# Kernel optimization log

Measured on AMD Instinct MI355X. Metric: run time of the kernel, lower is better.

## Reference

```python
import jax, jax.numpy as jnp
import numpy as np

EPS = 1e-6
B, N, K = 4, 65536, 16
D_IN, D_OUT, DH = 8, 16, 8  # DH = d_out // 2


def _bn(x, g, b):
    # train-mode BatchNorm2d over (B, N, K) per channel (channels-last here)
    m = jnp.mean(x, axis=(0, 1, 2))
    v = jnp.var(x, axis=(0, 1, 2))
    return (x - m) * jax.lax.rsqrt(v + EPS) * g + b


def _conv(x, w, b):
    # 1x1 Conv2d == per-point linear; x: (B,N,K,Cin), w: (Cout,Cin)
    return jnp.einsum('bnki,oi->bnko', x, w) + b


def _lse(coords, feats, idx, w, b, g, bt):
    # coords: (B,N,3), feats: (B,N,1,D), idx: (B,N,K)
    nbrs = jnp.take_along_axis(coords[:, :, None, :], idx[:, :, :, None], axis=1)  # (B,N,K,3)
    ctr = jnp.broadcast_to(coords[:, :, None, :], nbrs.shape)
    dist = jnp.ones(idx.shape + (1,), dtype=coords.dtype)  # torch path passes idx only -> dist = ones
    enc = jnp.concatenate([ctr, nbrs, ctr - nbrs, dist], axis=-1)  # (B,N,K,10)
    h = jax.nn.relu(_bn(_conv(enc, w, b), g, bt))
    f = jnp.broadcast_to(feats, idx.shape + (feats.shape[-1],))
    return jnp.concatenate([h, f], axis=-1)  # (B,N,K,2*D)


def _pool(x, sw, w, b, g, bt):
    # attentive pooling: softmax over neighbor axis K (axis=2)
    scores = jax.nn.softmax(jnp.einsum('bnki,oi->bnko', x, sw), axis=2)
    agg = jnp.sum(scores * x, axis=2, keepdims=True)  # (B,N,1,C)
    return jax.nn.relu(_bn(_conv(agg, w, b), g, bt))


def setup_inputs() -> dict:
    key = jax.random.key(0)
    ks = jax.random.split(key, 16)
    rn = lambda k, s: (0.1 * jax.random.normal(k, s)).astype(jnp.float32)
    inp = {
        'coords': jax.random.normal(ks[0], (B, N, 3), dtype=jnp.float32),
        'features': jax.random.normal(ks[1], (B, D_IN, N, 1), dtype=jnp.float32),
        'idx': jax.random.randint(ks[2], (B, N, K), 0, N, dtype=jnp.int32),
        # mlp1: d_in -> d_out//2, no bn, LeakyReLU(0.2)
        'w1': rn(ks[3], (DH, D_IN)), 'b1': jnp.zeros((DH,), jnp.float32),
        # lse1 mlp: 10 -> d_out//2, bn + ReLU
        'lse1_w': rn(ks[4], (DH, 10)), 'lse1_b': jnp.zeros((DH,), jnp.float32),
        'lse1_g': jnp.ones((DH,), jnp.float32), 'lse1_bt': jnp.zeros((DH,), jnp.float32),
        # pool1: in d_out -> out d_out//2
        'p1_sw': rn(ks[5], (D_OUT, D_OUT)),
        'p1_w': rn(ks[6], (DH, D_OUT)), 'p1_b': jnp.zeros((DH,), jnp.float32),
        'p1_g': jnp.ones((DH,), jnp.float32), 'p1_bt': jnp.zeros((DH,), jnp.float32),
        # lse2
        'lse2_w': rn(ks[7], (DH, 10)), 'lse2_b': jnp.zeros((DH,), jnp.float32),
        'lse2_g': jnp.ones((DH,), jnp.float32), 'lse2_bt': jnp.zeros((DH,), jnp.float32),
        # pool2: in d_out -> out d_out
        'p2_sw': rn(ks[8], (D_OUT, D_OUT)),
        'p2_w': rn(ks[9], (D_OUT, D_OUT)), 'p2_b': jnp.zeros((D_OUT,), jnp.float32),
        'p2_g': jnp.ones((D_OUT,), jnp.float32), 'p2_bt': jnp.zeros((D_OUT,), jnp.float32),
        # mlp2: d_out -> 2*d_out (no bn/act)
        'w2': rn(ks[10], (2 * D_OUT, D_OUT)), 'b2': jnp.zeros((2 * D_OUT,), jnp.float32),
        # shortcut: d_in -> 2*d_out, bn, no act
        'sc_w': rn(ks[11], (2 * D_OUT, D_IN)), 'sc_b': jnp.zeros((2 * D_OUT,), jnp.float32),
        'sc_g': jnp.ones((2 * D_OUT,), jnp.float32), 'sc_bt': jnp.zeros((2 * D_OUT,), jnp.float32),
    }
    return inp


def reference(coords, features, idx, w1, b1, lse1_w, lse1_b, lse1_g, lse1_bt,
              p1_sw, p1_w, p1_b, p1_g, p1_bt, lse2_w, lse2_b, lse2_g, lse2_bt,
              p2_sw, p2_w, p2_b, p2_g, p2_bt, w2, b2, sc_w, sc_b, sc_g, sc_bt):
    feats = jnp.transpose(features, (0, 2, 3, 1))  # (B,N,1,d_in) channels-last
    x = jax.nn.leaky_relu(_conv(feats, w1, b1), 0.2)           # (B,N,1,DH)
    x = _lse(coords, x, idx, lse1_w, lse1_b, lse1_g, lse1_bt)  # (B,N,K,D_OUT)
    x = _pool(x, p1_sw, p1_w, p1_b, p1_g, p1_bt)               # (B,N,1,DH)
    x = _lse(coords, x, idx, lse2_w, lse2_b, lse2_g, lse2_bt)  # (B,N,K,D_OUT)
    x = _pool(x, p2_sw, p2_w, p2_b, p2_g, p2_bt)               # (B,N,1,D_OUT)
    out = jax.nn.leaky_relu(
        _conv(x, w2, b2) + _bn(_conv(feats, sc_w, sc_b), sc_g, sc_bt), 0.01)
    return jnp.transpose(out, (0, 3, 1, 2))  # (B, 2*d_out, N, 1)
```

## Files before the change

kernel.cpp:

```cpp
#include <hip/hip_runtime.h>

#define NB 4
#define NN 65536
#define NK 16
#define NP (NB * NN)
#define BN_EPS 1e-6f
#define LOG2E 1.44269504088896f

#define WS_ENC_M   0
#define WS_SC_M    32
#define WS_S_Y2    96
#define WS_SS_Y2   104
#define WS_S_Y4    112
#define WS_SS_Y4   128
#define WS_Y2      1024
#define WS_Y4      (1024 + NP * 8)
#define WS_C4      (1024 + NP * 24)
#define WS_NB      (1024 + NP * 28)

template <int NCH>
__device__ inline void blockReduceAtomic(float (&v)[NCH], float* __restrict__ dst) {
    __shared__ float red[4][NCH];
    const int lane = threadIdx.x & 63;
    const int wv = threadIdx.x >> 6;
    __syncthreads();
#pragma unroll
    for (int c = 0; c < NCH; c++) {
        float x = v[c];
#pragma unroll
        for (int off = 32; off > 0; off >>= 1) x += __shfl_xor(x, off, 64);
        if (lane == 0) red[wv][c] = x;
    }
    __syncthreads();
    for (int c = threadIdx.x; c < NCH; c += 256)
        atomicAdd(dst + c, red[0][c] + red[1][c] + red[2][c] + red[3][c]);
    __syncthreads();
}

__device__ inline void bn_from_enc(const float* __restrict__ M, const float* __restrict__ w,
                                   float b, float g, float bt, float& sc, float& sh) {
    float u[6];
    u[0] = w[0] + w[6]; u[1] = w[1] + w[7]; u[2] = w[2] + w[8];
    u[3] = w[3] - w[6]; u[4] = w[4] - w[7]; u[5] = w[5] - w[8];
    const float beta = b + w[9];
    float lin = 0.f;
#pragma unroll
    for (int i = 0; i < 6; i++) lin += u[i] * M[i];
    float quad = u[0] * u[0] * M[6] + 2.f * u[0] * u[1] * M[7] + 2.f * u[0] * u[2] * M[8]
               + u[1] * u[1] * M[9] + 2.f * u[1] * u[2] * M[10] + u[2] * u[2] * M[11];
#pragma unroll
    for (int i = 0; i < 3; i++)
#pragma unroll
        for (int j = 0; j < 3; j++) quad += 2.f * u[i] * u[3 + j] * M[12 + i * 3 + j];
    quad += u[3] * u[3] * M[21] + 2.f * u[3] * u[4] * M[22] + 2.f * u[3] * u[5] * M[23]
          + u[4] * u[4] * M[24] + 2.f * u[4] * u[5] * M[25] + u[5] * u[5] * M[26];
    const float cnt = (float)NP * (float)NK;
    const float sum = lin + cnt * beta;
    const float ss = quad + 2.f * beta * lin + cnt * beta * beta;
    const float m = sum / cnt, v = ss / cnt - m * m;
    sc = g * rsqrtf(v + BN_EPS);
    sh = bt - m * sc;
}

__global__ __launch_bounds__(256) void k_pack(
    const float* __restrict__ coords, const float* __restrict__ feats,
    float4* __restrict__ c4, float* __restrict__ ws) {
    const int tid = threadIdx.x;
    const int p = blockIdx.x * 256 + tid;
    const int b = p >> 16;
    const int n = p & (NN - 1);
    c4[p] = make_float4(coords[3 * p], coords[3 * p + 1], coords[3 * p + 2], 0.f);
    float accf[44];
    float f[8];
#pragma unroll
    for (int i = 0; i < 8; i++) f[i] = feats[(b * 8 + i) * NN + n];
#pragma unroll
    for (int i = 0; i < 8; i++) accf[i] = f[i];
    int t2 = 8;
#pragma unroll
    for (int i = 0; i < 8; i++)
#pragma unroll
        for (int j = i; j < 8; j++) accf[t2++] = f[i] * f[j];
    blockReduceAtomic<44>(accf, ws + WS_SC_M);
}

__global__ __launch_bounds__(256) void k_stats(
    const float4* __restrict__ c4, const int* __restrict__ idx,
    float* __restrict__ ws) {
    const int tid = threadIdx.x;
    const int p = blockIdx.x * 256 + tid;
    const int b = p >> 16;
    const int boff = b << 16;
    float* __restrict__ nbp = ws + WS_NB;
    const int4* ip = (const int4*)idx + p * 4;
    const float4 me = c4[p];

    float sn0 = 0.f, sn1 = 0.f, sn2 = 0.f;
    float m00 = 0.f, m01 = 0.f, m02 = 0.f, m11 = 0.f, m12 = 0.f, m22 = 0.f;

    auto emit = [&](int k, const float4 nn) {
        nbp[(3 * k    ) * NP + p] = nn.x;
        nbp[(3 * k + 1) * NP + p] = nn.y;
        nbp[(3 * k + 2) * NP + p] = nn.z;
        sn0 += nn.x; sn1 += nn.y; sn2 += nn.z;
        m00 += nn.x * nn.x; m01 += nn.x * nn.y; m02 += nn.x * nn.z;
        m11 += nn.y * nn.y; m12 += nn.y * nn.z; m22 += nn.z * nn.z;
    };

    int4 v = ip[0];
    float4 n0 = c4[boff + v.x], n1 = c4[boff + v.y], n2 = c4[boff + v.z], n3 = c4[boff + v.w];
#pragma unroll 1
    for (int q = 0; q < 3; q++) {
        const int4 vn = ip[q + 1];
        const float4 t0 = c4[boff + vn.x], t1 = c4[boff + vn.y],
                     t2 = c4[boff + vn.z], t3 = c4[boff + vn.w];
        emit(4 * q, n0); emit(4 * q + 1, n1); emit(4 * q + 2, n2); emit(4 * q + 3, n3);
        n0 = t0; n1 = t1; n2 = t2; n3 = t3;
    }
    emit(12, n0); emit(13, n1); emit(14, n2); emit(15, n3);

    float acc[27];
    acc[0] = 16.f * me.x; acc[1] = 16.f * me.y; acc[2] = 16.f * me.z;
    acc[3] = sn0; acc[4] = sn1; acc[5] = sn2;
    acc[6] = 16.f * me.x * me.x; acc[7] = 16.f * me.x * me.y; acc[8] = 16.f * me.x * me.z;
    acc[9] = 16.f * me.y * me.y; acc[10] = 16.f * me.y * me.z; acc[11] = 16.f * me.z * me.z;
    acc[12] = me.x * sn0; acc[13] = me.x * sn1; acc[14] = me.x * sn2;
    acc[15] = me.y * sn0; acc[16] = me.y * sn1; acc[17] = me.y * sn2;
    acc[18] = me.z * sn0; acc[19] = me.z * sn1; acc[20] = me.z * sn2;
    acc[21] = m00; acc[22] = m01; acc[23] = m02;
    acc[24] = m11; acc[25] = m12; acc[26] = m22;
    blockReduceAtomic<27>(acc, ws + WS_ENC_M);
}

__global__ __launch_bounds__(256) void k_pool1(
    const float4* __restrict__ c4, const float* __restrict__ feats,
    const float* __restrict__ w1, const float* __restrict__ b1,
    const float* __restrict__ lse1_w, const float* __restrict__ lse1_b,
    const float* __restrict__ lse1_g, const float* __restrict__ lse1_bt,
    const float* __restrict__ lse2_w, const float* __restrict__ lse2_b,
    const float* __restrict__ lse2_g, const float* __restrict__ lse2_bt,
    const float* __restrict__ p1_sw, const float* __restrict__ p1_w,
    const float* __restrict__ p1_b,
    const float* __restrict__ p2_sw, const float* __restrict__ p2_w,
    const float* __restrict__ p2_b, float* __restrict__ ws) {
    __shared__ float an1[24], dcA[24], dkA[8], an2[24], dcB[24], dkB[8],
        sws1[64], sws2[64], pws1[128], pws2[256], pbs1[8], pbs2[16], w1s[64], b1s[8];
    const int tid = threadIdx.x;
    if (tid < 8) {
        const int c = tid;
        {
            const float* w = lse1_w + c * 10;
            float sc, sh;
            bn_from_enc(ws + WS_ENC_M, w, lse1_b[c], lse1_g[c], lse1_bt[c], sc, sh);
#pragma unroll
            for (int i = 0; i < 3; i++) {
                an1[c * 3 + i] = sc * (w[3 + i] - w[6 + i]);
                dcA[c * 3 + i] = sc * (w[i] + w[6 + i]);
            }
            dkA[c] = sc * (lse1_b[c] + w[9]) + sh;
        }
        {
            const float* w = lse2_w + c * 10;
            float sc, sh;
            bn_from_enc(ws + WS_ENC_M, w, lse2_b[c], lse2_g[c], lse2_bt[c], sc, sh);
#pragma unroll
            for (int i = 0; i < 3; i++) {
                an2[c * 3 + i] = sc * (w[3 + i] - w[6 + i]);
                dcB[c * 3 + i] = sc * (w[i] + w[6 + i]);
            }
            dkB[c] = sc * (lse2_b[c] + w[9]) + sh;
        }
        b1s[c] = b1[c]; pbs1[c] = p1_b[c];
    }
    if (tid < 16) pbs2[tid] = p2_b[tid];
    if (tid < 64) {
        w1s[tid] = w1[tid];
        sws1[tid] = p1_sw[(tid >> 3) * 16 + (tid & 7)] * LOG2E;
        sws2[tid] = p2_sw[(tid >> 3) * 16 + (tid & 7)] * LOG2E;
    }
    if (tid < 128) pws1[tid] = p1_w[tid];
    if (tid < 256) pws2[tid] = p2_w[tid];
    __syncthreads();

    const int p = blockIdx.x * 256 + tid;
    const int b = p >> 16;
    const int n = p & (NN - 1);
    const float* __restrict__ nbp = ws + WS_NB;
    const float4 me = c4[p];
    float d1[8], d2[8];
#pragma unroll
    for (int c = 0; c < 8; c++) {
        d1[c] = dcA[c * 3] * me.x + dcA[c * 3 + 1] * me.y + dcA[c * 3 + 2] * me.z + dkA[c];
        d2[c] = dcB[c * 3] * me.x + dcB[c * 3 + 1] * me.y + dcB[c * 3 + 2] * me.z + dkB[c];
    }
    float l1[8] = {}, a1[8] = {}, l2[8] = {}, a2[8] = {};

    auto proc = [&](float nx, float ny, float nz) {
        float h[8];
#pragma unroll
        for (int c = 0; c < 8; c++) {
            float y = an1[c * 3] * nx + an1[c * 3 + 1] * ny + an1[c * 3 + 2] * nz + d1[c];
            h[c] = y > 0.f ? y : 0.f;
        }
#pragma unroll
        for (int o = 0; o < 8; o++) {
            float s = 0.f;
#pragma unroll
            for (int i = 0; i < 8; i++) s += h[i] * sws1[o * 8 + i];
            float e2 = exp2f(s);
            l1[o] += e2; a1[o] += e2 * h[o];
        }
#pragma unroll
        for (int c = 0; c < 8; c++) {
            float y = an2[c * 3] * nx + an2[c * 3 + 1] * ny + an2[c * 3 + 2] * nz + d2[c];
            h[c] = y > 0.f ? y : 0.f;
        }
#pragma unroll
        for (int o = 0; o < 8; o++) {
            float s = 0.f;
#pragma unroll
            for (int i = 0; i < 8; i++) s += h[i] * sws2[o * 8 + i];
            float e2 = exp2f(s);
            l2[o] += e2; a2[o] += e2 * h[o];
        }
    };

    float X[4], Y[4], Z[4];
#pragma unroll
    for (int e = 0; e < 4; e++) {
        X[e] = nbp[(3 * e    ) * NP + p];
        Y[e] = nbp[(3 * e + 1) * NP + p];
        Z[e] = nbp[(3 * e + 2) * NP + p];
    }
#pragma unroll 1
    for (int q = 0; q < 3; q++) {
        float TX[4], TY[4], TZ[4];
#pragma unroll
        for (int e = 0; e < 4; e++) {
            const int k = 4 * (q + 1) + e;
            TX[e] = nbp[(3 * k    ) * NP + p];
            TY[e] = nbp[(3 * k + 1) * NP + p];
            TZ[e] = nbp[(3 * k + 2) * NP + p];
        }
#pragma unroll
        for (int e = 0; e < 4; e++) proc(X[e], Y[e], Z[e]);
#pragma unroll
        for (int e = 0; e < 4; e++) { X[e] = TX[e]; Y[e] = TY[e]; Z[e] = TZ[e]; }
    }
#pragma unroll
    for (int e = 0; e < 4; e++) proc(X[e], Y[e], Z[e]);

    float f[8];
#pragma unroll
    for (int i = 0; i < 8; i++) f[i] = feats[(b * 8 + i) * NN + n];
    float agg[16];
#pragma unroll
    for (int o = 0; o < 8; o++) agg[o] = a1[o] * __builtin_amdgcn_rcpf(l1[o]);
#pragma unroll
    for (int jq = 0; jq < 8; jq++) {
        float y = b1s[jq];
#pragma unroll
        for (int i = 0; i < 8; i++) y += f[i] * w1s[jq * 8 + i];
        agg[8 + jq] = y > 0.f ? y : 0.2f * y;
    }
    float st[16];
#pragma unroll
    for (int c = 0; c < 8; c++) {
        float y = pbs1[c];
#pragma unroll
        for (int o = 0; o < 16; o++) y += agg[o] * pws1[c * 16 + o];
        ws[WS_Y2 + c * NP + p] = y;
        st[c] = y; st[8 + c] = y * y;
    }
    float g2[8];
#pragma unroll
    for (int o = 0; o < 8; o++) g2[o] = a2[o] * __builtin_amdgcn_rcpf(l2[o]);
#pragma unroll
    for (int c = 0; c < 16; c++) {
        float y = pbs2[c];
#pragma unroll
        for (int o = 0; o < 8; o++) y += g2[o] * pws2[c * 16 + o];
        ws[WS_Y4 + c * NP + p] = y;
    }
    blockReduceAtomic<16>(st, ws + WS_S_Y2);
}

__global__ __launch_bounds__(256) void k_pool2e(
    const float* __restrict__ p1_g, const float* __restrict__ p1_bt,
    const float* __restrict__ p2_w, float* __restrict__ ws) {
    __shared__ float p1sc[8], p1sh[8], pwsb[128];
    const int tid = threadIdx.x;
    if (tid < 8) {
        const int c = tid;
        const float cP = 1.f / (float)NP;
        float m = ws[WS_S_Y2 + c] * cP, vv = ws[WS_SS_Y2 + c] * cP - m * m;
        float sc = p1_g[c] * rsqrtf(vv + BN_EPS);
        p1sc[c] = sc; p1sh[c] = p1_bt[c] - m * sc;
    }
    if (tid < 128) pwsb[tid] = p2_w[(tid >> 3) * 16 + 8 + (tid & 7)];
    __syncthreads();

    const int p = blockIdx.x * 256 + tid;
    float x2[8];
#pragma unroll
    for (int c = 0; c < 8; c++) {
        float y = ws[WS_Y2 + c * NP + p] * p1sc[c] + p1sh[c];
        x2[c] = y > 0.f ? y : 0.f;
    }
    float st[32];
#pragma unroll
    for (int c = 0; c < 16; c++) {
        float y = ws[WS_Y4 + c * NP + p];
#pragma unroll
        for (int o = 0; o < 8; o++) y += x2[o] * pwsb[c * 8 + o];
        ws[WS_Y4 + c * NP + p] = y;
        st[c] = y; st[16 + c] = y * y;
    }
    blockReduceAtomic<32>(st, ws + WS_S_Y4);
}

__global__ __launch_bounds__(256) void k_final(
    const float* __restrict__ feats, const float* __restrict__ w2,
    const float* __restrict__ b2, const float* __restrict__ sc_w,
    const float* __restrict__ sc_b, const float* __restrict__ p2_g,
    const float* __restrict__ p2_bt, const float* __restrict__ sc_g,
    const float* __restrict__ sc_bt, const float* __restrict__ ws,
    float* __restrict__ out) {
    __shared__ float w2s[512], b2s[32], scws[256], scbs[32],
        p2sc[16], p2sh[16], scsc[32], scsh[32];
    const int tid = threadIdx.x;
    for (int i = tid; i < 512; i += 256) w2s[i] = w2[i];
    if (tid < 256) scws[tid] = sc_w[tid];
    if (tid < 32) {
        b2s[tid] = b2[tid]; scbs[tid] = sc_b[tid];
        const int c = tid;
        const float* w = sc_w + c * 8;
        const float* S = ws + WS_SC_M;
        float lin = 0.f;
#pragma unroll
        for (int i = 0; i < 8; i++) lin += w[i] * S[i];
        float quad = 0.f;
        int t2 = 0;
#pragma unroll
        for (int i = 0; i < 8; i++)
#pragma unroll
            for (int j = i; j < 8; j++) {
                const float mm = S[8 + t2++];
                quad += (i == j ? 1.f : 2.f) * w[i] * w[j] * mm;
            }
        const float cnt = (float)NP;
        const float bb = sc_b[c];
        const float sum = lin + cnt * bb;
        const float ss = quad + 2.f * bb * lin + cnt * bb * bb;
        const float m = sum / cnt, vv = ss / cnt - m * m;
        const float sc = sc_g[c] * rsqrtf(vv + BN_EPS);
        scsc[c] = sc; scsh[c] = sc_bt[c] - m * sc;
    }
    if (tid < 16) {
        const int c = tid;
        const float cP = 1.f / (float)NP;
        float m = ws[WS_S_Y4 + c] * cP, vv = ws[WS_SS_Y4 + c] * cP - m * m;
        float sc = p2_g[c] * rsqrtf(vv + BN_EPS);
        p2sc[c] = sc; p2sh[c] = p2_bt[c] - m * sc;
    }
    __syncthreads();

    const int p = blockIdx.x * 256 + tid;
    const int b = p >> 16;
    const int n = p & (NN - 1);
    float x4[16];
#pragma unroll
    for (int c = 0; c < 16; c++) {
        float y = ws[WS_Y4 + c * NP + p] * p2sc[c] + p2sh[c];
        x4[c] = y > 0.f ? y : 0.f;
    }
    float f[8];
#pragma unroll
    for (int i = 0; i < 8; i++) f[i] = feats[(b * 8 + i) * NN + n];
#pragma unroll
    for (int c = 0; c < 32; c++) {
        float s = scbs[c];
#pragma unroll
        for (int i = 0; i < 8; i++) s += f[i] * scws[c * 8 + i];
        s = s * scsc[c] + scsh[c];
        float m = b2s[c];
#pragma unroll
        for (int o = 0; o < 16; o++) m += x4[o] * w2s[c * 16 + o];
        float vv = m + s;
        out[(b * 32 + c) * NN + n] = vv > 0.f ? vv : 0.01f * vv;
    }
}

extern "C" void kernel_launch(void* const* d_in, const int* in_sizes, int n_in,
                              void* d_out, int out_size, void* d_ws, size_t ws_size,
                              hipStream_t stream) {
    (void)in_sizes; (void)n_in; (void)out_size; (void)ws_size;
    const float* coords = (const float*)d_in[0];
    const float* features = (const float*)d_in[1];
    const int* idx = (const int*)d_in[2];
    const float* w1 = (const float*)d_in[3];
    const float* b1 = (const float*)d_in[4];
    const float* lse1_w = (const float*)d_in[5];
    const float* lse1_b = (const float*)d_in[6];
    const float* lse1_g = (const float*)d_in[7];
    const float* lse1_bt = (const float*)d_in[8];
    const float* p1_sw = (const float*)d_in[9];
    const float* p1_w = (const float*)d_in[10];
    const float* p1_b = (const float*)d_in[11];
    const float* p1_g = (const float*)d_in[12];
    const float* p1_bt = (const float*)d_in[13];
    const float* lse2_w = (const float*)d_in[14];
    const float* lse2_b = (const float*)d_in[15];
    const float* lse2_g = (const float*)d_in[16];
    const float* lse2_bt = (const float*)d_in[17];
    const float* p2_sw = (const float*)d_in[18];
    const float* p2_w = (const float*)d_in[19];
    const float* p2_b = (const float*)d_in[20];
    const float* p2_g = (const float*)d_in[21];
    const float* p2_bt = (const float*)d_in[22];
    const float* w2 = (const float*)d_in[23];
    const float* b2 = (const float*)d_in[24];
    const float* sc_w = (const float*)d_in[25];
    const float* sc_b = (const float*)d_in[26];
    const float* sc_g = (const float*)d_in[27];
    const float* sc_bt = (const float*)d_in[28];
    float* ws = (float*)d_ws;
    float* out = (float*)d_out;
    float4* c4 = (float4*)(ws + WS_C4);

    const int NBLK = NP / 256;
    (void)hipMemsetAsync(ws, 0, 144 * sizeof(float), stream);
    k_pack<<<NBLK, 256, 0, stream>>>(coords, features, c4, ws);
    k_stats<<<NBLK, 256, 0, stream>>>(c4, idx, ws);
    k_pool1<<<NBLK, 256, 0, stream>>>(c4, features, w1, b1,
                                      lse1_w, lse1_b, lse1_g, lse1_bt,
                                      lse2_w, lse2_b, lse2_g, lse2_bt,
                                      p1_sw, p1_w, p1_b, p2_sw, p2_w, p2_b, ws);
    k_pool2e<<<NBLK, 256, 0, stream>>>(p1_g, p1_bt, p2_w, ws);
    k_final<<<NBLK, 256, 0, stream>>>(features, w2, b2, sc_w, sc_b, p2_g, p2_bt,
                                      sc_g, sc_bt, ws, out);
}
```

Before: 339.4 us.

## Split fused pool kernel into two passes and pack workspace as float4

The combined pool kernel, which evaluated both LSE/attention branches per neighbor, is split into two kernels that each handle one branch, with launch bounds requesting higher occupancy. The gathered neighbor coordinates and the Y2/Y4 intermediates are repacked so each thread moves 16-byte float4s instead of scalar channel planes. exp2f is replaced by the hardware exp2 builtin. In exchange, the neighbor buffer is read twice and an extra launch is added, aiming to cut register pressure and memory instructions.

```diff
diff --git a/kernel.cpp b/kernel.cpp
--- a/kernel.cpp
+++ b/kernel.cpp
@@ -13,10 +13,10 @@
 #define WS_SS_Y2   104
 #define WS_S_Y4    112
 #define WS_SS_Y4   128
-#define WS_Y2      1024
-#define WS_Y4      (1024 + NP * 8)
-#define WS_C4      (1024 + NP * 24)
-#define WS_NB      (1024 + NP * 28)
+#define WS_C4      1024
+#define WS_NB4     (1024 + NP * 4)
+#define WS_Y2      (1024 + NP * 52)
+#define WS_Y4      (1024 + NP * 60)
 
 template <int NCH>
 __device__ inline void blockReduceAtomic(float (&v)[NCH], float* __restrict__ dst) {
@@ -91,20 +91,23 @@
     const int p = blockIdx.x * 256 + tid;
     const int b = p >> 16;
     const int boff = b << 16;
-    float* __restrict__ nbp = ws + WS_NB;
+    float4* __restrict__ nb4 = (float4*)(ws + WS_NB4);
     const int4* ip = (const int4*)idx + p * 4;
     const float4 me = c4[p];
 
     float sn0 = 0.f, sn1 = 0.f, sn2 = 0.f;
     float m00 = 0.f, m01 = 0.f, m02 = 0.f, m11 = 0.f, m12 = 0.f, m22 = 0.f;
 
-    auto emit = [&](int k, const float4 nn) {
-        nbp[(3 * k    ) * NP + p] = nn.x;
-        nbp[(3 * k + 1) * NP + p] = nn.y;
-        nbp[(3 * k + 2) * NP + p] = nn.z;
+    auto mom = [&](const float4 nn) {
         sn0 += nn.x; sn1 += nn.y; sn2 += nn.z;
         m00 += nn.x * nn.x; m01 += nn.x * nn.y; m02 += nn.x * nn.z;
         m11 += nn.y * nn.y; m12 += nn.y * nn.z; m22 += nn.z * nn.z;
+    };
+    auto emitq = [&](int q, const float4 n0, const float4 n1, const float4 n2, const float4 n3) {
+        nb4[(3 * q    ) * NP + p] = make_float4(n0.x, n0.y, n0.z, n1.x);
+        nb4[(3 * q + 1) * NP + p] = make_float4(n1.y, n1.z, n2.x, n2.y);
+        nb4[(3 * q + 2) * NP + p] = make_float4(n2.z, n3.x, n3.y, n3.z);
+        mom(n0); mom(n1); mom(n2); mom(n3);
     };
 
     int4 v = ip[0];
@@ -114,10 +117,10 @@
         const int4 vn = ip[q + 1];
         const float4 t0 = c4[boff + vn.x], t1 = c4[boff + vn.y],
                      t2 = c4[boff + vn.z], t3 = c4[boff + vn.w];
-        emit(4 * q, n0); emit(4 * q + 1, n1); emit(4 * q + 2, n2); emit(4 * q + 3, n3);
+        emitq(q, n0, n1, n2, n3);
         n0 = t0; n1 = t1; n2 = t2; n3 = t3;
     }
-    emit(12, n0); emit(13, n1); emit(14, n2); emit(15, n3);
+    emitq(3, n0, n1, n2, n3);
 
     float acc[27];
     acc[0] = 16.f * me.x; acc[1] = 16.f * me.y; acc[2] = 16.f * me.z;
@@ -132,68 +135,45 @@
     blockReduceAtomic<27>(acc, ws + WS_ENC_M);
 }
 
-__global__ __launch_bounds__(256) void k_pool1(
+__global__ __launch_bounds__(256, 3) void k_pool1a(
     const float4* __restrict__ c4, const float* __restrict__ feats,
     const float* __restrict__ w1, const float* __restrict__ b1,
     const float* __restrict__ lse1_w, const float* __restrict__ lse1_b,
     const float* __restrict__ lse1_g, const float* __restrict__ lse1_bt,
-    const float* __restrict__ lse2_w, const float* __restrict__ lse2_b,
-    const float* __restrict__ lse2_g, const float* __restrict__ lse2_bt,
     const float* __restrict__ p1_sw, const float* __restrict__ p1_w,
-    const float* __restrict__ p1_b,
-    const float* __restrict__ p2_sw, const float* __restrict__ p2_w,
-    const float* __restrict__ p2_b, float* __restrict__ ws) {
-    __shared__ float an1[24], dcA[24], dkA[8], an2[24], dcB[24], dkB[8],
-        sws1[64], sws2[64], pws1[128], pws2[256], pbs1[8], pbs2[16], w1s[64], b1s[8];
+    const float* __restrict__ p1_b, float* __restrict__ ws) {
+    __shared__ float an1[24], dcA[24], dkA[8], sws1[64], pws1[128], pbs1[8], w1s[64], b1s[8];
     const int tid = threadIdx.x;
     if (tid < 8) {
         const int c = tid;
-        {
-            const float* w = lse1_w + c * 10;
-            float sc, sh;
-            bn_from_enc(ws + WS_ENC_M, w, lse1_b[c], lse1_g[c], lse1_bt[c], sc, sh);
-#pragma unroll
-            for (int i = 0; i < 3; i++) {
-                an1[c * 3 + i] = sc * (w[3 + i] - w[6 + i]);
-                dcA[c * 3 + i] = sc * (w[i] + w[6 + i]);
-            }
-            dkA[c] = sc * (lse1_b[c] + w[9]) + sh;
-        }
-        {
-            const float* w = lse2_w + c * 10;
-            float sc, sh;
-            bn_from_enc(ws + WS_ENC_M, w, lse2_b[c], lse2_g[c], lse2_bt[c], sc, sh);
-#pragma unroll
-            for (int i = 0; i < 3; i++) {
-                an2[c * 3 + i] = sc * (w[3 + i] - w[6 + i]);
-                dcB[c * 3 + i] = sc * (w[i] + w[6 + i]);
-            }
-            dkB[c] = sc * (lse2_b[c] + w[9]) + sh;
-        }
+        const float* w = lse1_w + c * 10;
+        float sc, sh;
+        bn_from_enc(ws + WS_ENC_M, w, lse1_b[c], lse1_g[c], lse1_bt[c], sc, sh);
+#pragma unroll
+        for (int i = 0; i < 3; i++) {
+            an1[c * 3 + i] = sc * (w[3 + i] - w[6 + i]);
+            dcA[c * 3 + i] = sc * (w[i] + w[6 + i]);
+        }
+        dkA[c] = sc * (lse1_b[c] + w[9]) + sh;
         b1s[c] = b1[c]; pbs1[c] = p1_b[c];
     }
-    if (tid < 16) pbs2[tid] = p2_b[tid];
     if (tid < 64) {
         w1s[tid] = w1[tid];
         sws1[tid] = p1_sw[(tid >> 3) * 16 + (tid & 7)] * LOG2E;
-        sws2[tid] = p2_sw[(tid >> 3) * 16 + (tid & 7)] * LOG2E;
     }
     if (tid < 128) pws1[tid] = p1_w[tid];
-    if (tid < 256) pws2[tid] = p2_w[tid];
     __syncthreads();
 
     const int p = blockIdx.x * 256 + tid;
     const int b = p >> 16;
     const int n = p & (NN - 1);
-    const float* __restrict__ nbp = ws + WS_NB;
+    const float4* __restrict__ nb4 = (const float4*)(ws + WS_NB4);
     const float4 me = c4[p];
-    float d1[8], d2[8];
-#pragma unroll
-    for (int c = 0; c < 8; c++) {
+    float d1[8];
+#pragma unroll
+    for (int c = 0; c < 8; c++)
         d1[c] = dcA[c * 3] * me.x + dcA[c * 3 + 1] * me.y + dcA[c * 3 + 2] * me.z + dkA[c];
-        d2[c] = dcB[c * 3] * me.x + dcB[c * 3 + 1] * me.y + dcB[c * 3 + 2] * me.z + dkB[c];
-    }
-    float l1[8] = {}, a1[8] = {}, l2[8] = {}, a2[8] = {};
+    float l1[8] = {}, a1[8] = {};
 
     auto proc = [&](float nx, float ny, float nz) {
         float h[8];
@@ -207,9 +187,88 @@
             float s = 0.f;
 #pragma unroll
             for (int i = 0; i < 8; i++) s += h[i] * sws1[o * 8 + i];
-            float e2 = exp2f(s);
+            float e2 = __builtin_amdgcn_exp2f(s);
             l1[o] += e2; a1[o] += e2 * h[o];
         }
+    };
+    auto proc4 = [&](const float4 c0, const float4 c1, const float4 c2) {
+        proc(c0.x, c0.y, c0.z); proc(c0.w, c1.x, c1.y);
+        proc(c1.z, c1.w, c2.x); proc(c2.y, c2.z, c2.w);
+    };
+
+    float4 A0 = nb4[0 * NP + p], A1 = nb4[1 * NP + p], A2 = nb4[2 * NP + p];
+#pragma unroll 1
+    for (int g = 0; g < 3; g++) {
+        const float4 B0 = nb4[(3 * g + 3) * NP + p], B1 = nb4[(3 * g + 4) * NP + p],
+                     B2 = nb4[(3 * g + 5) * NP + p];
+        proc4(A0, A1, A2);
+        A0 = B0; A1 = B1; A2 = B2;
+    }
+    proc4(A0, A1, A2);
+
+    float f[8];
+#pragma unroll
+    for (int i = 0; i < 8; i++) f[i] = feats[(b * 8 + i) * NN + n];
+    float agg[16];
+#pragma unroll
+    for (int o = 0; o < 8; o++) agg[o] = a1[o] * __builtin_amdgcn_rcpf(l1[o]);
+#pragma unroll
+    for (int jq = 0; jq < 8; jq++) {
+        float y = b1s[jq];
+#pragma unroll
+        for (int i = 0; i < 8; i++) y += f[i] * w1s[jq * 8 + i];
+        agg[8 + jq] = y > 0.f ? y : 0.2f * y;
+    }
+    float st[16], yv[8];
+#pragma unroll
+    for (int c = 0; c < 8; c++) {
+        float y = pbs1[c];
+#pragma unroll
+        for (int o = 0; o < 16; o++) y += agg[o] * pws1[c * 16 + o];
+        yv[c] = y; st[c] = y; st[8 + c] = y * y;
+    }
+    float4* __restrict__ y2 = (float4*)(ws + WS_Y2);
+    y2[0 * NP + p] = make_float4(yv[0], yv[1], yv[2], yv[3]);
+    y2[1 * NP + p] = make_float4(yv[4], yv[5], yv[6], yv[7]);
+    blockReduceAtomic<16>(st, ws + WS_S_Y2);
+}
+
+__global__ __launch_bounds__(256, 3) void k_pool1b(
+    const float4* __restrict__ c4,
+    const float* __restrict__ lse2_w, const float* __restrict__ lse2_b,
+    const float* __restrict__ lse2_g, const float* __restrict__ lse2_bt,
+    const float* __restrict__ p2_sw, const float* __restrict__ p2_w,
+    const float* __restrict__ p2_b, float* __restrict__ ws) {
+    __shared__ float an2[24], dcB[24], dkB[8], sws2[64], pws2h[128], pbs2[16];
+    const int tid = threadIdx.x;
+    if (tid < 8) {
+        const int c = tid;
+        const float* w = lse2_w + c * 10;
+        float sc, sh;
+        bn_from_enc(ws + WS_ENC_M, w, lse2_b[c], lse2_g[c], lse2_bt[c], sc, sh);
+#pragma unroll
+        for (int i = 0; i < 3; i++) {
+            an2[c * 3 + i] = sc * (w[3 + i] - w[6 + i]);
+            dcB[c * 3 + i] = sc * (w[i] + w[6 + i]);
+        }
+        dkB[c] = sc * (lse2_b[c] + w[9]) + sh;
+    }
+    if (tid < 16) pbs2[tid] = p2_b[tid];
+    if (tid < 64) sws2[tid] = p2_sw[(tid >> 3) * 16 + (tid & 7)] * LOG2E;
+    if (tid < 128) pws2h[tid] = p2_w[(tid >> 3) * 16 + (tid & 7)];
+    __syncthreads();
+
+    const int p = blockIdx.x * 256 + tid;
+    const float4* __restrict__ nb4 = (const float4*)(ws + WS_NB4);
+    const float4 me = c4[p];
+    float d2[8];
+#pragma unroll
+    for (int c = 0; c < 8; c++)
+        d2[c] = dcB[c * 3] * me.x + dcB[c * 3 + 1] * me.y + dcB[c * 3 + 2] * me.z + dkB[c];
+    float l2[8] = {}, a2[8] = {};
+
+    auto proc = [&](float nx, float ny, float nz) {
+        float h[8];
 #pragma unroll
         for (int c = 0; c < 8; c++) {
             float y = an2[c * 3] * nx + an2[c * 3 + 1] * ny + an2[c * 3 + 2] * nz + d2[c];
@@ -220,69 +279,42 @@
             float s = 0.f;
 #pragma unroll
             for (int i = 0; i < 8; i++) s += h[i] * sws2[o * 8 + i];
-            float e2 = exp2f(s);
+            float e2 = __builtin_amdgcn_exp2f(s);
             l2[o] += e2; a2[o] += e2 * h[o];
         }
     };
-
-    float X[4], Y[4], Z[4];
-#pragma unroll
-    for (int e = 0; e < 4; e++) {
-        X[e] = nbp[(3 * e    ) * NP + p];
-        Y[e] = nbp[(3 * e + 1) * NP + p];
-        Z[e] = nbp[(3 * e + 2) * NP + p];
-    }
+    auto proc4 = [&](const float4 c0, const float4 c1, const float4 c2) {
+        proc(c0.x, c0.y, c0.z); proc(c0.w, c1.x, c1.y);
+        proc(c1.z, c1.w, c2.x); proc(c2.y, c2.z, c2.w);
+    };
+
+    float4 A0 = nb4[0 * NP + p], A1 = nb4[1 * NP + p], A2 = nb4[2 * NP + p];
 #pragma unroll 1
-    for (int q = 0; q < 3; q++) {
-        float TX[4], TY[4], TZ[4];
-#pragma unroll
-        for (int e = 0; e < 4; e++) {
-            const int k = 4 * (q + 1) + e;
-            TX[e] = nbp[(3 * k    ) * NP + p];
-            TY[e] = nbp[(3 * k + 1) * NP + p];
-            TZ[e] = nbp[(3 * k + 2) * NP + p];
-        }
-#pragma unroll
-        for (int e = 0; e < 4; e++) proc(X[e], Y[e], Z[e]);
-#pragma unroll
-        for (int e = 0; e < 4; e++) { X[e] = TX[e]; Y[e] = TY[e]; Z[e] = TZ[e]; }
-    }
-#pragma unroll
-    for (int e = 0; e < 4; e++) proc(X[e], Y[e], Z[e]);
-
-    float f[8];
-#pragma unroll
-    for (int i = 0; i < 8; i++) f[i] = feats[(b * 8 + i) * NN + n];
-    float agg[16];
-#pragma unroll
-    for (int o = 0; o < 8; o++) agg[o] = a1[o] * __builtin_amdgcn_rcpf(l1[o]);
-#pragma unroll
-    for (int jq = 0; jq < 8; jq++) {
-        float y = b1s[jq];
-#pragma unroll
-        for (int i = 0; i < 8; i++) y += f[i] * w1s[jq * 8 + i];
-        agg[8 + jq] = y > 0.f ? y : 0.2f * y;
-    }
-    float st[16];
-#pragma unroll
-    for (int c = 0; c < 8; c++) {
-        float y = pbs1[c];
-#pragma unroll
-        for (int o = 0; o < 16; o++) y += agg[o] * pws1[c * 16 + o];
-        ws[WS_Y2 + c * NP + p] = y;
-        st[c] = y; st[8 + c] = y * y;
-    }
+    for (int g = 0; g < 3; g++) {
+        const float4 B0 = nb4[(3 * g + 3) * NP + p], B1 = nb4[(3 * g + 4) * NP + p],
+                     B2 = nb4[(3 * g + 5) * NP + p];
+        proc4(A0, A1, A2);
+        A0 = B0; A1 = B1; A2 = B2;
+    }
+    proc4(A0, A1, A2);
+
     float g2[8];
 #pragma unroll
     for (int o = 0; o < 8; o++) g2[o] = a2[o] * __builtin_amdgcn_rcpf(l2[o]);
-#pragma unroll
-    for (int c = 0; c < 16; c++) {
-        float y = pbs2[c];
-#pragma unroll
-        for (int o = 0; o < 8; o++) y += g2[o] * pws2[c * 16 + o];
-        ws[WS_Y4 + c * NP + p] = y;
-    }
-    blockReduceAtomic<16>(st, ws + WS_S_Y2);
+    float4* __restrict__ y4 = (float4*)(ws + WS_Y4);
+#pragma unroll
+    for (int cq = 0; cq < 4; cq++) {
+        float yv[4];
+#pragma unroll
+        for (int j = 0; j < 4; j++) {
+            const int c = cq * 4 + j;
+            float y = pbs2[c];
+#pragma unroll
+            for (int o = 0; o < 8; o++) y += g2[o] * pws2h[c * 8 + o];
+            yv[j] = y;
+        }
+        y4[cq * NP + p] = make_float4(yv[0], yv[1], yv[2], yv[3]);
+    }
 }
 
 __global__ __launch_bounds__(256) void k_pool2e(
@@ -301,20 +333,29 @@
     __syncthreads();
 
     const int p = blockIdx.x * 256 + tid;
-    float x2[8];
+    const float4* __restrict__ y2 = (const float4*)(ws + WS_Y2);
+    float4* __restrict__ y4 = (float4*)(ws + WS_Y4);
+    const float4 v0 = y2[0 * NP + p], v1 = y2[1 * NP + p];
+    float x2[8] = {v0.x, v0.y, v0.z, v0.w, v1.x, v1.y, v1.z, v1.w};
 #pragma unroll
     for (int c = 0; c < 8; c++) {
-        float y = ws[WS_Y2 + c * NP + p] * p1sc[c] + p1sh[c];
+        float y = x2[c] * p1sc[c] + p1sh[c];
         x2[c] = y > 0.f ? y : 0.f;
     }
     float st[32];
 #pragma unroll
-    for (int c = 0; c < 16; c++) {
-        float y = ws[WS_Y4 + c * NP + p];
-#pragma unroll
-        for (int o = 0; o < 8; o++) y += x2[o] * pwsb[c * 8 + o];
-        ws[WS_Y4 + c * NP + p] = y;
-        st[c] = y; st[16 + c] = y * y;
+    for (int cq = 0; cq < 4; cq++) {
+        float4 v = y4[cq * NP + p];
+        float yv[4] = {v.x, v.y, v.z, v.w};
+#pragma unroll
+        for (int j = 0; j < 4; j++) {
+            const int c = cq * 4 + j;
+            float y = yv[j];
+#pragma unroll
+            for (int o = 0; o < 8; o++) y += x2[o] * pwsb[c * 8 + o];
+            yv[j] = y; st[c] = y; st[16 + c] = y * y;
+        }
+        y4[cq * NP + p] = make_float4(yv[0], yv[1], yv[2], yv[3]);
     }
     blockReduceAtomic<32>(st, ws + WS_S_Y4);
 }
@@ -368,11 +409,18 @@
     const int p = blockIdx.x * 256 + tid;
     const int b = p >> 16;
     const int n = p & (NN - 1);
+    const float4* __restrict__ y4 = (const float4*)(ws + WS_Y4);
     float x4[16];
 #pragma unroll
-    for (int c = 0; c < 16; c++) {
-        float y = ws[WS_Y4 + c * NP + p] * p2sc[c] + p2sh[c];
-        x4[c] = y > 0.f ? y : 0.f;
+    for (int cq = 0; cq < 4; cq++) {
+        const float4 v = y4[cq * NP + p];
+        const float yv[4] = {v.x, v.y, v.z, v.w};
+#pragma unroll
+        for (int j = 0; j < 4; j++) {
+            const int c = cq * 4 + j;
+            float y = yv[j] * p2sc[c] + p2sh[c];
+            x4[c] = y > 0.f ? y : 0.f;
+        }
     }
     float f[8];
 #pragma unroll
@@ -432,10 +480,11 @@
     (void)hipMemsetAsync(ws, 0, 144 * sizeof(float), stream);
     k_pack<<<NBLK, 256, 0, stream>>>(coords, features, c4, ws);
     k_stats<<<NBLK, 256, 0, stream>>>(c4, idx, ws);
-    k_pool1<<<NBLK, 256, 0, stream>>>(c4, features, w1, b1,
-                                      lse1_w, lse1_b, lse1_g, lse1_bt,
-                                      lse2_w, lse2_b, lse2_g, lse2_bt,
-                                      p1_sw, p1_w, p1_b, p2_sw, p2_w, p2_b, ws);
+    k_pool1a<<<NBLK, 256, 0, stream>>>(c4, features, w1, b1,
+                                       lse1_w, lse1_b, lse1_g, lse1_bt,
+                                       p1_sw, p1_w, p1_b, ws);
+    k_pool1b<<<NBLK, 256, 0, stream>>>(c4, lse2_w, lse2_b, lse2_g, lse2_bt,
+                                       p2_sw, p2_w, p2_b, ws);
     k_pool2e<<<NBLK, 256, 0, stream>>>(p1_g, p1_bt, p2_w, ws);
     k_final<<<NBLK, 256, 0, stream>>>(features, w2, b2, sc_w, sc_b, p2_g, p2_bt,
                                       sc_g, sc_bt, ws, out);
```

Measured after the change: 468.4 us. 38.0% more time.
